# Performance work log

Hardware: AMD Instinct MI355X
Metric: run time of the kernel (lower is better)

## Reference

```python
import jax, jax.numpy as jnp
import numpy as np

NUM_SYM = 50000
NUM_HERB = 50000
N_NODES = NUM_SYM + NUM_HERB
DIM = 128
N_EDGES = 3200000
N_LAYERS = 2


def setup_inputs() -> dict:
    key = jax.random.key(0)
    k1, k2, k3, k4, k5 = jax.random.split(key, 5)
    sym_emb = jax.random.normal(k1, (NUM_SYM, DIM), dtype=jnp.float32)
    herb_emb = jax.random.normal(k2, (NUM_HERB, DIM), dtype=jnp.float32)
    adj_rows = jax.random.randint(k3, (N_EDGES,), 0, N_NODES, dtype=jnp.int32)
    adj_cols = jax.random.randint(k4, (N_EDGES,), 0, N_NODES, dtype=jnp.int32)
    # normalized-Laplacian values are positive; uniform stands in for D^-1/2 A D^-1/2 entries
    adj_vals = jax.random.uniform(k5, (N_EDGES,), dtype=jnp.float32)
    return {"sym_emb": sym_emb, "herb_emb": herb_emb,
            "adj_rows": adj_rows, "adj_cols": adj_cols, "adj_vals": adj_vals}


def _spmm(rows, cols, vals, x):
    # sparse [N,N] @ dense [N,D]: gather source rows, scale, scatter-add to dest rows
    msgs = vals[:, None] * x[cols]              # [E, D]
    return jax.ops.segment_sum(msgs, rows, num_segments=N_NODES)


def reference(sym_emb, herb_emb, adj_rows, adj_cols, adj_vals):
    ego = jnp.concatenate([sym_emb, herb_emb], axis=0)   # [N, D]
    acc = ego
    e = ego
    for _ in range(N_LAYERS):
        e = _spmm(adj_rows, adj_cols, adj_vals, e)
        acc = acc + e
    all_emb = acc / jnp.float32(N_LAYERS + 1)            # mean over stacked layers
    return all_emb[:NUM_SYM], all_emb[NUM_SYM:]
```

## Files before the change

kernel.cpp:

```cpp
#include <hip/hip_runtime.h>

#define NUM_SYM 50000
#define NUM_HERB 50000
#define N_NODES (NUM_SYM + NUM_HERB)
#define DIM 128
#define NB_BUCKETS ((N_NODES + 255) / 256)
#define CHUNK 4096
#define NG 8
#define PAD 16

typedef float floatx4 __attribute__((ext_vector_type(4)));

__device__ __forceinline__ float bf2f(unsigned short u) {
    return __uint_as_float((unsigned)u << 16);
}
__device__ __forceinline__ unsigned short f2bf(float f) {
    unsigned u = __float_as_uint(f);
    unsigned r = (u + 0x7FFFu + ((u >> 16) & 1u)) >> 16;
    return (unsigned short)r;
}

__global__ __launch_bounds__(256) void to_bf16(
    const float* __restrict__ sym, const float* __restrict__ herb,
    ushort* __restrict__ xbf)
{
    int i = blockIdx.x * 256 + threadIdx.x;
    const int n4 = N_NODES * DIM / 4;
    if (i >= n4) return;
    const int sym4 = NUM_SYM * DIM / 4;
    float4 v = (i < sym4) ? reinterpret_cast<const float4*>(sym)[i]
                          : reinterpret_cast<const float4*>(herb)[i - sym4];
    ushort4 o;
    o.x = f2bf(v.x); o.y = f2bf(v.y); o.z = f2bf(v.z); o.w = f2bf(v.w);
    reinterpret_cast<ushort4*>(xbf)[i] = o;
}


__global__ __launch_bounds__(1024) void scatter_slots(
    const int* __restrict__ rows, const int* __restrict__ cols,
    const float* __restrict__ vals, int E, int CAP, int SUBCAP,
    int* __restrict__ cur, int2* __restrict__ slots)
{
    __shared__ int lh[NB_BUCKETS];
    __shared__ int labs[NB_BUCKETS];
    for (int i = threadIdx.x; i < NB_BUCKETS; i += 1024) lh[i] = 0;
    __syncthreads();
    int g = blockIdx.x & (NG - 1);
    int start = blockIdx.x * CHUNK;
    int end   = min(start + CHUNK, E);
    for (int e = start + threadIdx.x; e < end; e += 1024)
        atomicAdd(&lh[rows[e] >> 8], 1);
    __syncthreads();
    for (int i = threadIdx.x; i < NB_BUCKETS; i += 1024) {
        int c = lh[i];
        int resv = c ? atomicAdd(&cur[(i * NG + g) * PAD], c) : 0;
        labs[i] = i * CAP + g * SUBCAP + resv;
        lh[i] = 0;
    }
    __syncthreads();
    for (int e = start + threadIdx.x; e < end; e += 1024) {
        int r = rows[e];
        int key = r >> 8;
        int pos = labs[key] + atomicAdd(&lh[key], 1);
        slots[pos] = make_int2(((r & 255) << 17) | cols[e],
                               __float_as_int(vals[e]));
    }
}

__global__ __launch_bounds__(1024) void slots_to_csr(
    const int2* __restrict__ slots, const int* __restrict__ cur,
    int CAP, int SUBCAP,
    int* __restrict__ csr, int* __restrict__ rowptr, int* __restrict__ rowend)
{
    __shared__ int h[256];
    __shared__ int cnt[NG];
    int b = blockIdx.x, t = threadIdx.x;
    if (t < NG) cnt[t] = cur[(b * NG + t) * PAD];
    if (t < 256) h[t] = 0;
    __syncthreads();
    size_t sb = (size_t)b * CAP;
    for (int g = 0; g < NG; ++g) {
        int n = cnt[g];
        const int2* p = slots + sb + (size_t)g * SUBCAP;
        for (int j = t; j < n; j += 1024)
            atomicAdd(&h[(unsigned)p[j].x >> 17], 1);
    }
    __syncthreads();
    int v = (t < 256) ? h[t] : 0;
    for (int o = 1; o < 256; o <<= 1) {
        int x = (t < 256 && t >= o) ? h[t - o] : 0;
        __syncthreads();
        if (t < 256) h[t] += x;
        __syncthreads();
    }
    int cb = b * CAP;
    if (t < 256) {
        int r = b * 256 + t;
        if (r < N_NODES) {
            rowptr[r] = cb + (h[t] - v);
            rowend[r] = cb + h[t];
        }
    }
    __syncthreads();
    if (t < 256) h[t] -= v;
    __syncthreads();
    for (int g = 0; g < NG; ++g) {
        int n = cnt[g];
        const int2* p = slots + sb + (size_t)g * SUBCAP;
        for (int j = t; j < n; j += 1024) {
            int2 rec = p[j];
            int key = (unsigned)rec.x >> 17;
            int pos = cb + atomicAdd(&h[key], 1);
            unsigned vb = (unsigned)f2bf(__int_as_float(rec.y));
            csr[pos] = (int)((vb << 17) | ((unsigned)rec.x & 0x1FFFFu));
        }
    }
}

__device__ __forceinline__ float unpack_val(int p) {
    return __uint_as_float(((unsigned)p >> 17) << 16);
}

template <bool FUSE_MEAN>
__global__ __launch_bounds__(256) void spmm_csr_bf16(
    const int* __restrict__ csr, const int* __restrict__ rowptr,
    const int* __restrict__ rowend,
    const ushort* __restrict__ xbf,
    const float* __restrict__ sym, const float* __restrict__ herb,
    const ushort* __restrict__ e1bf,
    void* __restrict__ outp)
{
    int wave = blockIdx.x * 4 + (threadIdx.x >> 6);
    int half = (threadIdx.x >> 5) & 1;
    int lane = threadIdx.x & 31;
    int r = wave * 2 + half;
    if (r >= N_NODES) return;

    int j   = rowptr[r];
    int end = rowend[r];

    float4 acc = make_float4(0.f, 0.f, 0.f, 0.f);
    for (; j + 7 < end; j += 8) {
        int p0 = csr[j], p1 = csr[j + 1], p2 = csr[j + 2], p3 = csr[j + 3];
        int p4 = csr[j + 4], p5 = csr[j + 5], p6 = csr[j + 6], p7 = csr[j + 7];
        ushort4 m0 = reinterpret_cast<const ushort4*>(xbf + (size_t)(p0 & 0x1FFFF) * DIM)[lane];
        ushort4 m1 = reinterpret_cast<const ushort4*>(xbf + (size_t)(p1 & 0x1FFFF) * DIM)[lane];
        ushort4 m2 = reinterpret_cast<const ushort4*>(xbf + (size_t)(p2 & 0x1FFFF) * DIM)[lane];
        ushort4 m3 = reinterpret_cast<const ushort4*>(xbf + (size_t)(p3 & 0x1FFFF) * DIM)[lane];
        ushort4 m4 = reinterpret_cast<const ushort4*>(xbf + (size_t)(p4 & 0x1FFFF) * DIM)[lane];
        ushort4 m5 = reinterpret_cast<const ushort4*>(xbf + (size_t)(p5 & 0x1FFFF) * DIM)[lane];
        ushort4 m6 = reinterpret_cast<const ushort4*>(xbf + (size_t)(p6 & 0x1FFFF) * DIM)[lane];
        ushort4 m7 = reinterpret_cast<const ushort4*>(xbf + (size_t)(p7 & 0x1FFFF) * DIM)[lane];
        float v0 = unpack_val(p0), v1 = unpack_val(p1);
        float v2 = unpack_val(p2), v3 = unpack_val(p3);
        float v4 = unpack_val(p4), v5 = unpack_val(p5);
        float v6 = unpack_val(p6), v7 = unpack_val(p7);
        acc.x += v0 * bf2f(m0.x) + v1 * bf2f(m1.x) + v2 * bf2f(m2.x) + v3 * bf2f(m3.x)
               + v4 * bf2f(m4.x) + v5 * bf2f(m5.x) + v6 * bf2f(m6.x) + v7 * bf2f(m7.x);
        acc.y += v0 * bf2f(m0.y) + v1 * bf2f(m1.y) + v2 * bf2f(m2.y) + v3 * bf2f(m3.y)
               + v4 * bf2f(m4.y) + v5 * bf2f(m5.y) + v6 * bf2f(m6.y) + v7 * bf2f(m7.y);
        acc.z += v0 * bf2f(m0.z) + v1 * bf2f(m1.z) + v2 * bf2f(m2.z) + v3 * bf2f(m3.z)
               + v4 * bf2f(m4.z) + v5 * bf2f(m5.z) + v6 * bf2f(m6.z) + v7 * bf2f(m7.z);
        acc.w += v0 * bf2f(m0.w) + v1 * bf2f(m1.w) + v2 * bf2f(m2.w) + v3 * bf2f(m3.w)
               + v4 * bf2f(m4.w) + v5 * bf2f(m5.w) + v6 * bf2f(m6.w) + v7 * bf2f(m7.w);
    }
    for (; j + 3 < end; j += 4) {
        int p0 = csr[j], p1 = csr[j + 1], p2 = csr[j + 2], p3 = csr[j + 3];
        ushort4 m0 = reinterpret_cast<const ushort4*>(xbf + (size_t)(p0 & 0x1FFFF) * DIM)[lane];
        ushort4 m1 = reinterpret_cast<const ushort4*>(xbf + (size_t)(p1 & 0x1FFFF) * DIM)[lane];
        ushort4 m2 = reinterpret_cast<const ushort4*>(xbf + (size_t)(p2 & 0x1FFFF) * DIM)[lane];
        ushort4 m3 = reinterpret_cast<const ushort4*>(xbf + (size_t)(p3 & 0x1FFFF) * DIM)[lane];
        float v0 = unpack_val(p0), v1 = unpack_val(p1);
        float v2 = unpack_val(p2), v3 = unpack_val(p3);
        acc.x += v0 * bf2f(m0.x) + v1 * bf2f(m1.x) + v2 * bf2f(m2.x) + v3 * bf2f(m3.x);
        acc.y += v0 * bf2f(m0.y) + v1 * bf2f(m1.y) + v2 * bf2f(m2.y) + v3 * bf2f(m3.y);
        acc.z += v0 * bf2f(m0.z) + v1 * bf2f(m1.z) + v2 * bf2f(m2.z) + v3 * bf2f(m3.z);
        acc.w += v0 * bf2f(m0.w) + v1 * bf2f(m1.w) + v2 * bf2f(m2.w) + v3 * bf2f(m3.w);
    }
    for (; j < end; ++j) {
        int p0 = csr[j];
        float v0 = unpack_val(p0);
        ushort4 m0 = reinterpret_cast<const ushort4*>(xbf + (size_t)(p0 & 0x1FFFF) * DIM)[lane];
        acc.x += v0 * bf2f(m0.x);
        acc.y += v0 * bf2f(m0.y);
        acc.z += v0 * bf2f(m0.z);
        acc.w += v0 * bf2f(m0.w);
    }

    if (FUSE_MEAN) {
        const float4* egorow = (r < NUM_SYM)
            ? reinterpret_cast<const float4*>(sym  + (size_t)r * DIM)
            : reinterpret_cast<const float4*>(herb + (size_t)(r - NUM_SYM) * DIM);
        float4 g = egorow[lane];
        ushort4 a = reinterpret_cast<const ushort4*>(e1bf + (size_t)r * DIM)[lane];
        const float s = 1.0f / 3.0f;
        floatx4 o;
        o.x = (g.x + bf2f(a.x) + acc.x) * s;
        o.y = (g.y + bf2f(a.y) + acc.y) * s;
        o.z = (g.z + bf2f(a.z) + acc.z) * s;
        o.w = (g.w + bf2f(a.w) + acc.w) * s;
        __builtin_nontemporal_store(o,
            reinterpret_cast<floatx4*>((float*)outp + (size_t)r * DIM) + lane);
    } else {
        ushort4 o;
        o.x = f2bf(acc.x); o.y = f2bf(acc.y); o.z = f2bf(acc.z); o.w = f2bf(acc.w);
        reinterpret_cast<ushort4*>((ushort*)outp + (size_t)r * DIM)[lane] = o;
    }
}

__global__ __launch_bounds__(256) void spmm_scatter(
    const int* __restrict__ rows, const int* __restrict__ cols,
    const float* __restrict__ vals, int n_edges,
    const float* __restrict__ xa, const float* __restrict__ xb,
    float* __restrict__ out)
{
    int gid = blockIdx.x * 256 + threadIdx.x;
    int edge = gid >> 5;
    if (edge >= n_edges) return;
    int sub = gid & 31;
    int c = cols[edge];
    int r = rows[edge];
    float v = vals[edge];
    const float* xrow = (c < NUM_SYM) ? (xa + (size_t)c * DIM)
                                      : (xb + (size_t)(c - NUM_SYM) * DIM);
    float4 m = reinterpret_cast<const float4*>(xrow)[sub];
    float* o = out + (size_t)r * DIM + (size_t)sub * 4;
    unsafeAtomicAdd(o + 0, v * m.x);
    unsafeAtomicAdd(o + 1, v * m.y);
    unsafeAtomicAdd(o + 2, v * m.z);
    unsafeAtomicAdd(o + 3, v * m.w);
}

__global__ __launch_bounds__(256) void finalize_mean(
    const float* __restrict__ sym, const float* __restrict__ herb,
    const float* __restrict__ e1, float* __restrict__ out)
{
    int i = blockIdx.x * 256 + threadIdx.x;
    const int n4 = N_NODES * DIM / 4;
    if (i >= n4) return;
    const int sym4 = NUM_SYM * DIM / 4;
    float4 e = (i < sym4) ? reinterpret_cast<const float4*>(sym)[i]
                          : reinterpret_cast<const float4*>(herb)[i - sym4];
    float4 a = reinterpret_cast<const float4*>(e1)[i];
    float4 b = reinterpret_cast<float4*>(out)[i];
    const float s = 1.0f / 3.0f;
    float4 r;
    r.x = (e.x + a.x + b.x) * s;
    r.y = (e.y + a.y + b.y) * s;
    r.z = (e.z + a.z + b.z) * s;
    r.w = (e.w + a.w + b.w) * s;
    reinterpret_cast<float4*>(out)[i] = r;
}

extern "C" void kernel_launch(void* const* d_in, const int* in_sizes, int n_in,
                              void* d_out, int out_size, void* d_ws, size_t ws_size,
                              hipStream_t stream) {
    const float* sym  = (const float*)d_in[0];
    const float* herb = (const float*)d_in[1];
    const int*   rows = (const int*)d_in[2];
    const int*   cols = (const int*)d_in[3];
    const float* vals = (const float*)d_in[4];
    const int E = in_sizes[2];
    float* out = (float*)d_out;

    int CAP = (int)(((long)E / NB_BUCKETS) * 5 / 4);
    CAP = (CAP + NG * 32 - 1) / (NG * 32) * (NG * 32);
    if (CAP < NG * 64) CAP = NG * 64;
    const int SUBCAP = CAP / NG;

    char* ws = (char*)d_ws;
    auto align256 = [](size_t x) { return (x + 255) & ~(size_t)255; };
    const size_t xbf_bytes   = (size_t)N_NODES * DIM * sizeof(ushort);
    const size_t csr_off     = align256(xbf_bytes);
    const size_t slot_off    = align256(csr_off + (size_t)NB_BUCKETS * CAP * 4);
    const size_t slot_bytes  = (size_t)NB_BUCKETS * CAP * 8 > xbf_bytes
                             ? (size_t)NB_BUCKETS * CAP * 8 : xbf_bytes;
    const size_t rowptr_off  = align256(slot_off + slot_bytes);
    const size_t rowend_off  = align256(rowptr_off + (size_t)N_NODES * 4);
    const size_t cur_off     = align256(rowend_off + (size_t)N_NODES * 4);
    const size_t required    = cur_off + (size_t)NB_BUCKETS * NG * PAD * 4;

    if (ws_size < required || E >= (1 << 22)) {
        float* e1 = (float*)ws;
        const size_t e1_bytes = (size_t)N_NODES * DIM * sizeof(float);
        hipMemsetAsync(e1, 0, e1_bytes, stream);
        hipMemsetAsync(out, 0, e1_bytes, stream);
        const int spmm_blocks = (E * 32 + 255) / 256;
        spmm_scatter<<<spmm_blocks, 256, 0, stream>>>(rows, cols, vals, E, sym, herb, e1);
        spmm_scatter<<<spmm_blocks, 256, 0, stream>>>(rows, cols, vals, E,
                                                      e1, e1 + (size_t)NUM_SYM * DIM, out);
        const int n4 = N_NODES * DIM / 4;
        finalize_mean<<<(n4 + 255) / 256, 256, 0, stream>>>(sym, herb, e1, out);
        return;
    }

    ushort* xbf    = (ushort*)ws;
    int*    csr    = (int*)(ws + csr_off);
    int2*   slots  = (int2*)(ws + slot_off);
    ushort* e1bf   = (ushort*)(ws + slot_off);
    int*    rowptr = (int*)(ws + rowptr_off);
    int*    rowend = (int*)(ws + rowend_off);
    int*    cur    = (int*)(ws + cur_off);

    hipMemsetAsync(cur, 0, (size_t)NB_BUCKETS * NG * PAD * 4, stream);
    const int EB = (E + CHUNK - 1) / CHUNK;
    scatter_slots<<<EB, 1024, 0, stream>>>(rows, cols, vals, E, CAP, SUBCAP, cur, slots);
    slots_to_csr<<<NB_BUCKETS, 1024, 0, stream>>>(slots, cur, CAP, SUBCAP,
                                                  csr, rowptr, rowend);

    const int n4 = N_NODES * DIM / 4;
    to_bf16<<<(n4 + 255) / 256, 256, 0, stream>>>(sym, herb, xbf);

    const int blocks = (N_NODES / 2 + 3) / 4;
    spmm_csr_bf16<false><<<blocks, 256, 0, stream>>>(csr, rowptr, rowend, xbf,
                                                     nullptr, nullptr, nullptr, e1bf);
    spmm_csr_bf16<true><<<blocks, 256, 0, stream>>>(csr, rowptr, rowend, e1bf,
                                                    sym, herb, e1bf, out);
}
```

Baseline: 424.4 us.

## Merge bf16 conversion into scatter kernel and shrink buckets to 128 rows

Folds the fp32-to-bf16 embedding conversion into the edge scatter kernel as extra blocks, which removes one launch and lets the conversion overlap with the scatter. Buckets shrink from 256 to 128 rows, and the per-bucket sub-group split (NG) is dropped, so each bucket has one atomic cursor and one contiguous slot region. The CAP slack factor goes from 5/4 to 9/8, and the workspace is reordered so slots come before csr. Removing NG puts more global atomic contention on each cursor. The smaller slack also raises the risk that a bucket overflows its capacity.

```diff
diff --git a/kernel.cpp b/kernel.cpp
--- a/kernel.cpp
+++ b/kernel.cpp
@@ -4,9 +4,8 @@
 #define NUM_HERB 50000
 #define N_NODES (NUM_SYM + NUM_HERB)
 #define DIM 128
-#define NB_BUCKETS ((N_NODES + 255) / 256)
+#define NB ((N_NODES + 127) / 128)
 #define CHUNK 4096
-#define NG 8
 #define PAD 16
 
 typedef float floatx4 __attribute__((ext_vector_type(4)));
@@ -20,100 +19,86 @@
     return (unsigned short)r;
 }
 
-__global__ __launch_bounds__(256) void to_bf16(
+__global__ __launch_bounds__(1024) void scatter_and_convert(
+    const int* __restrict__ rows, const int* __restrict__ cols,
+    const float* __restrict__ vals, int E, int CAP, int EB,
     const float* __restrict__ sym, const float* __restrict__ herb,
-    ushort* __restrict__ xbf)
-{
-    int i = blockIdx.x * 256 + threadIdx.x;
-    const int n4 = N_NODES * DIM / 4;
-    if (i >= n4) return;
-    const int sym4 = NUM_SYM * DIM / 4;
-    float4 v = (i < sym4) ? reinterpret_cast<const float4*>(sym)[i]
-                          : reinterpret_cast<const float4*>(herb)[i - sym4];
-    ushort4 o;
-    o.x = f2bf(v.x); o.y = f2bf(v.y); o.z = f2bf(v.z); o.w = f2bf(v.w);
-    reinterpret_cast<ushort4*>(xbf)[i] = o;
-}
-
-
-__global__ __launch_bounds__(1024) void scatter_slots(
-    const int* __restrict__ rows, const int* __restrict__ cols,
-    const float* __restrict__ vals, int E, int CAP, int SUBCAP,
-    int* __restrict__ cur, int2* __restrict__ slots)
-{
-    __shared__ int lh[NB_BUCKETS];
-    __shared__ int labs[NB_BUCKETS];
-    for (int i = threadIdx.x; i < NB_BUCKETS; i += 1024) lh[i] = 0;
-    __syncthreads();
-    int g = blockIdx.x & (NG - 1);
+    int* __restrict__ cur, int2* __restrict__ slots, ushort* __restrict__ xbf)
+{
+    __shared__ int lh[NB];
+    __shared__ int labs[NB];
+    if ((int)blockIdx.x >= EB) {
+        int i = ((int)blockIdx.x - EB) * 1024 + threadIdx.x;
+        const int n4 = N_NODES * DIM / 4;
+        if (i >= n4) return;
+        const int sym4 = NUM_SYM * DIM / 4;
+        float4 v = (i < sym4) ? reinterpret_cast<const float4*>(sym)[i]
+                              : reinterpret_cast<const float4*>(herb)[i - sym4];
+        ushort4 o;
+        o.x = f2bf(v.x); o.y = f2bf(v.y); o.z = f2bf(v.z); o.w = f2bf(v.w);
+        reinterpret_cast<ushort4*>(xbf)[i] = o;
+        return;
+    }
+    for (int i = threadIdx.x; i < NB; i += 1024) lh[i] = 0;
+    __syncthreads();
     int start = blockIdx.x * CHUNK;
     int end   = min(start + CHUNK, E);
     for (int e = start + threadIdx.x; e < end; e += 1024)
-        atomicAdd(&lh[rows[e] >> 8], 1);
-    __syncthreads();
-    for (int i = threadIdx.x; i < NB_BUCKETS; i += 1024) {
+        atomicAdd(&lh[rows[e] >> 7], 1);
+    __syncthreads();
+    for (int i = threadIdx.x; i < NB; i += 1024) {
         int c = lh[i];
-        int resv = c ? atomicAdd(&cur[(i * NG + g) * PAD], c) : 0;
-        labs[i] = i * CAP + g * SUBCAP + resv;
+        int resv = c ? atomicAdd(&cur[i * PAD], c) : 0;
+        labs[i] = i * CAP + resv;
         lh[i] = 0;
     }
     __syncthreads();
     for (int e = start + threadIdx.x; e < end; e += 1024) {
         int r = rows[e];
-        int key = r >> 8;
-        int pos = labs[key] + atomicAdd(&lh[key], 1);
-        slots[pos] = make_int2(((r & 255) << 17) | cols[e],
+        int k = r >> 7;
+        int pos = labs[k] + atomicAdd(&lh[k], 1);
+        slots[pos] = make_int2(((r & 127) << 17) | cols[e],
                                __float_as_int(vals[e]));
     }
 }
 
 __global__ __launch_bounds__(1024) void slots_to_csr(
-    const int2* __restrict__ slots, const int* __restrict__ cur,
-    int CAP, int SUBCAP,
+    const int2* __restrict__ slots, const int* __restrict__ cur, int CAP,
     int* __restrict__ csr, int* __restrict__ rowptr, int* __restrict__ rowend)
 {
-    __shared__ int h[256];
-    __shared__ int cnt[NG];
+    __shared__ int h[128];
     int b = blockIdx.x, t = threadIdx.x;
-    if (t < NG) cnt[t] = cur[(b * NG + t) * PAD];
-    if (t < 256) h[t] = 0;
-    __syncthreads();
+    int n = cur[b * PAD];
     size_t sb = (size_t)b * CAP;
-    for (int g = 0; g < NG; ++g) {
-        int n = cnt[g];
-        const int2* p = slots + sb + (size_t)g * SUBCAP;
-        for (int j = t; j < n; j += 1024)
-            atomicAdd(&h[(unsigned)p[j].x >> 17], 1);
-    }
-    __syncthreads();
-    int v = (t < 256) ? h[t] : 0;
-    for (int o = 1; o < 256; o <<= 1) {
-        int x = (t < 256 && t >= o) ? h[t - o] : 0;
+    if (t < 128) h[t] = 0;
+    __syncthreads();
+    for (int j = t; j < n; j += 1024)
+        atomicAdd(&h[(unsigned)slots[sb + j].x >> 17], 1);
+    __syncthreads();
+    int v = (t < 128) ? h[t] : 0;
+    for (int o = 1; o < 128; o <<= 1) {
+        int x = (t < 128 && t >= o) ? h[t - o] : 0;
         __syncthreads();
-        if (t < 256) h[t] += x;
+        if (t < 128) h[t] += x;
         __syncthreads();
     }
     int cb = b * CAP;
-    if (t < 256) {
-        int r = b * 256 + t;
+    if (t < 128) {
+        int r = b * 128 + t;
         if (r < N_NODES) {
             rowptr[r] = cb + (h[t] - v);
             rowend[r] = cb + h[t];
         }
     }
     __syncthreads();
-    if (t < 256) h[t] -= v;
-    __syncthreads();
-    for (int g = 0; g < NG; ++g) {
-        int n = cnt[g];
-        const int2* p = slots + sb + (size_t)g * SUBCAP;
-        for (int j = t; j < n; j += 1024) {
-            int2 rec = p[j];
-            int key = (unsigned)rec.x >> 17;
-            int pos = cb + atomicAdd(&h[key], 1);
-            unsigned vb = (unsigned)f2bf(__int_as_float(rec.y));
-            csr[pos] = (int)((vb << 17) | ((unsigned)rec.x & 0x1FFFFu));
-        }
+    if (t < 128) h[t] -= v;
+    __syncthreads();
+    for (int j = t; j < n; j += 1024) {
+        int2 rec = slots[sb + j];
+        int bin = (unsigned)rec.x >> 17;
+        int pos = cb + atomicAdd(&h[bin], 1);
+        unsigned vb = (unsigned)f2bf(__int_as_float(rec.y));
+        csr[pos] = (int)((vb << 17) | ((unsigned)rec.x & 0x1FFFFu));
     }
 }
 
@@ -263,22 +248,21 @@
     const int E = in_sizes[2];
     float* out = (float*)d_out;
 
-    int CAP = (int)(((long)E / NB_BUCKETS) * 5 / 4);
-    CAP = (CAP + NG * 32 - 1) / (NG * 32) * (NG * 32);
-    if (CAP < NG * 64) CAP = NG * 64;
-    const int SUBCAP = CAP / NG;
+    int CAP = (int)(((long)E / NB) * 9 / 8);
+    CAP = (CAP + 31) / 32 * 32;
+    if (CAP < 512) CAP = 512;
 
     char* ws = (char*)d_ws;
     auto align256 = [](size_t x) { return (x + 255) & ~(size_t)255; };
-    const size_t xbf_bytes   = (size_t)N_NODES * DIM * sizeof(ushort);
-    const size_t csr_off     = align256(xbf_bytes);
-    const size_t slot_off    = align256(csr_off + (size_t)NB_BUCKETS * CAP * 4);
-    const size_t slot_bytes  = (size_t)NB_BUCKETS * CAP * 8 > xbf_bytes
-                             ? (size_t)NB_BUCKETS * CAP * 8 : xbf_bytes;
-    const size_t rowptr_off  = align256(slot_off + slot_bytes);
-    const size_t rowend_off  = align256(rowptr_off + (size_t)N_NODES * 4);
-    const size_t cur_off     = align256(rowend_off + (size_t)N_NODES * 4);
-    const size_t required    = cur_off + (size_t)NB_BUCKETS * NG * PAD * 4;
+    const size_t xbf_bytes  = (size_t)N_NODES * DIM * sizeof(ushort);
+    const size_t slot_off   = align256(xbf_bytes);
+    const size_t slot_bytes = (size_t)NB * CAP * 8 > xbf_bytes
+                            ? (size_t)NB * CAP * 8 : xbf_bytes;
+    const size_t csr_off    = align256(slot_off + slot_bytes);
+    const size_t rowptr_off = align256(csr_off + (size_t)NB * CAP * 4);
+    const size_t rowend_off = align256(rowptr_off + (size_t)N_NODES * 4);
+    const size_t cur_off    = align256(rowend_off + (size_t)N_NODES * 4);
+    const size_t required   = cur_off + (size_t)NB * PAD * 4;
 
     if (ws_size < required || E >= (1 << 22)) {
         float* e1 = (float*)ws;
@@ -295,21 +279,21 @@
     }
 
     ushort* xbf    = (ushort*)ws;
-    int*    csr    = (int*)(ws + csr_off);
     int2*   slots  = (int2*)(ws + slot_off);
     ushort* e1bf   = (ushort*)(ws + slot_off);
+    int*    csr    = (int*)(ws + csr_off);
     int*    rowptr = (int*)(ws + rowptr_off);
     int*    rowend = (int*)(ws + rowend_off);
     int*    cur    = (int*)(ws + cur_off);
 
-    hipMemsetAsync(cur, 0, (size_t)NB_BUCKETS * NG * PAD * 4, stream);
-    const int EB = (E + CHUNK - 1) / CHUNK;
-    scatter_slots<<<EB, 1024, 0, stream>>>(rows, cols, vals, E, CAP, SUBCAP, cur, slots);
-    slots_to_csr<<<NB_BUCKETS, 1024, 0, stream>>>(slots, cur, CAP, SUBCAP,
-                                                  csr, rowptr, rowend);
-
-    const int n4 = N_NODES * DIM / 4;
-    to_bf16<<<(n4 + 255) / 256, 256, 0, stream>>>(sym, herb, xbf);
+    hipMemsetAsync(cur, 0, (size_t)NB * PAD * 4, stream);
+    const int EB   = (E + CHUNK - 1) / CHUNK;
+    const int n4   = N_NODES * DIM / 4;
+    const int CONV = (n4 + 1023) / 1024;
+    scatter_and_convert<<<EB + CONV, 1024, 0, stream>>>(rows, cols, vals, E, CAP, EB,
+                                                        sym, herb, cur, slots, xbf);
+
+    slots_to_csr<<<NB, 1024, 0, stream>>>(slots, cur, CAP, csr, rowptr, rowend);
 
     const int blocks = (N_NODES / 2 + 3) / 4;
     spmm_csr_bf16<false><<<blocks, 256, 0, stream>>>(csr, rowptr, rowend, xbf,
```

New measurement: 432.0 us. About the same (+1.8%).
